# Kernel optimization log

Measured on AMD Instinct MI355X. Metric: run time of the kernel, lower is better.

The kernel has to match this reference:

```python
import jax, jax.numpy as jnp
import numpy as np
from jax import lax

DN = ('NCH', 'OIH', 'NCH')

def _conv(x, w, b, pad):
    # x: [B, C, L]; replication (edge) pad then VALID conv, per nn.ReplicationPad1d + Conv1d
    if pad != (0, 0):
        x = jnp.pad(x, ((0, 0), (0, 0), pad), mode='edge')
    y = lax.conv_general_dilated(x, w, (1,), 'VALID', dimension_numbers=DN)
    return y + b[None, :, None]

def setup_inputs() -> dict:
    key = jax.random.key(0)
    ks = jax.random.split(key, 11)
    B, L, C, H = 32, 512, 300, 512
    s = 1.0 / np.sqrt(C)
    inp = {
        'x': jax.random.normal(ks[0], (B, L, C), jnp.float32),
        'w1': jax.random.normal(ks[1], (C, C, 1), jnp.float32) * s,
        'b1': jax.random.normal(ks[2], (C,), jnp.float32) * s,
        'w2': jax.random.normal(ks[3], (C, C, 2), jnp.float32) * s,
        'b2': jax.random.normal(ks[4], (C,), jnp.float32) * s,
        'w3': jax.random.normal(ks[5], (C, C, 3), jnp.float32) * s,
        'b3': jax.random.normal(ks[6], (C,), jnp.float32) * s,
        'w7': jax.random.normal(ks[7], (C, C, 7), jnp.float32) * s,
        'b7': jax.random.normal(ks[8], (C,), jnp.float32) * s,
        'slp_w': jax.random.normal(ks[9], (H, 5 * C), jnp.float32) * (1.0 / np.sqrt(5 * C)),
        'slp_b': jax.random.normal(ks[10], (H,), jnp.float32) * (1.0 / np.sqrt(5 * C)),
    }
    return inp

def reference(x, w1, b1, w2, b2, w3, b3, w7, b7, slp_w, slp_b):
    xc = jnp.transpose(x, (0, 2, 1))  # [B, C, L]
    x1 = jnp.tanh(_conv(xc, w1, b1, (0, 0)))
    x2 = jnp.tanh(_conv(xc, w2, b2, (0, 1)))
    x3 = jnp.tanh(_conv(xc, w3, b3, (1, 1)))
    x5 = x3  # faithful to the original bug: x5 = self.conv3(x)
    x7 = jnp.tanh(_conv(xc, w7, b7, (3, 3)))
    # concat channels -> [B, L, 1500], then linear + tanh -> [B, L, 512]
    h = jnp.concatenate([x1, x2, x3, x5, x7], axis=1)  # [B, 5C, L]
    h = jnp.transpose(h, (0, 2, 1))  # [B, L, 5C]
    out = jnp.tanh(jnp.einsum('blc,hc->blh', h, slp_w) + slp_b)
    return out
```

## Files before the change

kernel.cpp:

```cpp
#include <hip/hip_runtime.h>
#include <hip/hip_bf16.h>

typedef __attribute__((ext_vector_type(8))) short short8;
typedef __attribute__((ext_vector_type(16))) float floatx16;

#define Bn 32
#define Ln 512
#define Cn 300
#define Hn 512
#define Nn (Bn*Ln)
#define XBP 518
#define XBC 320
#define HK 1216
#define LDSTC 72

#define XROWS 134
#define XSZ (XROWS*LDSTC)
#define HSROWS 128
#define HSSZ (HSROWS*LDSTC)

#define XB_ELEMS (Bn*XBP*XBC)
#define WB_ELEMS 1597440
#define WC_ELEMS (Hn*HK)
#define XB_OFF 0
#define WB_OFF (XB_OFF + XB_ELEMS)
#define WC_OFF (WB_OFF + WB_ELEMS)
#define HB_OFF (WC_OFF + WC_ELEMS)

__device__ __forceinline__ float fast_tanh(float x) {
    float ax = __builtin_fabsf(x);
    float t  = __expf(-2.f * ax);
    float r  = __builtin_fmaf(-2.f * t, __frcp_rn(1.f + t), 1.f);
    return __builtin_copysignf(r, x);
}

__device__ __forceinline__ short f2bf(float v) {
    __hip_bfloat16 h = __float2bfloat16(v);
    return *reinterpret_cast<short*>(&h);
}

__global__ void prep_all(const float* __restrict__ x,
                         const float* __restrict__ w1, const float* __restrict__ w2,
                         const float* __restrict__ w3, const float* __restrict__ w7,
                         const float* __restrict__ slp_w,
                         __hip_bfloat16* __restrict__ wsb) {
    int g = blockIdx.x * 256 + threadIdx.x;
    int idx = g * 8;
    short8 o;
    if (idx < XB_ELEMS) {
        int c8 = idx % XBC;
        int t  = idx / XBC;
        int p = t % XBP;
        int b = t / XBP;
        int l = p - 3;
        l = l < 0 ? 0 : (l > Ln - 1 ? Ln - 1 : l);
        const float* row = x + (b * Ln + l) * Cn;
        if (c8 + 8 <= Cn) {
            float4 a = *(const float4*)(row + c8);
            float4 bq = *(const float4*)(row + c8 + 4);
            o[0] = f2bf(a.x); o[1] = f2bf(a.y); o[2] = f2bf(a.z); o[3] = f2bf(a.w);
            o[4] = f2bf(bq.x); o[5] = f2bf(bq.y); o[6] = f2bf(bq.z); o[7] = f2bf(bq.w);
        } else {
#pragma unroll
            for (int e = 0; e < 8; ++e) {
                int c = c8 + e;
                o[e] = f2bf(c < Cn ? row[c] : 0.f);
            }
        }
        *(short8*)&wsb[idx] = o;
    } else if (idx < WB_OFF + WB_ELEMS) {
        int r = idx - WB_OFF, taps; const float* w;
        if (r < 122880)       { taps = 1; w = w1; }
        else if (r < 368640)  { taps = 2; w = w2; r -= 122880; }
        else if (r < 737280)  { taps = 3; w = w3; r -= 368640; }
        else                  { taps = 7; w = w7; r -= 737280; }
        int lane = (r >> 3) & 63;
        int f    = (r >> 9) & 15;
        int rt   = r >> 13;
        int t    = rt % taps;
        int mc   = rt / taps;
        int ch   = mc % 5;
        int mt   = mc / 5;
        int ks = f >> 2, mq = f & 3;
        int m = mt * 128 + mq * 32 + (lane & 31);
        int cb = ch * 64 + ks * 16 + (lane >> 5) * 8;
#pragma unroll
        for (int e = 0; e < 8; ++e) {
            int c = cb + e;
            o[e] = f2bf((m < Cn && c < Cn) ? w[(m * Cn + c) * taps + t] : 0.f);
        }
        *(short8*)&wsb[idx] = o;
    } else if (idx < WC_OFF + WC_ELEMS) {
        int r = idx - WC_OFF;
        int lane = (r >> 3) & 63;
        int f    = (r >> 9) & 15;
        int mc   = r >> 13;
        int ch   = mc % 19;
        int mt4  = mc / 19;
        int ks = f >> 2, mq = f & 3;
        int h = mt4 * 128 + mq * 32 + (lane & 31);
        int kb = ch * 64 + ks * 16 + (lane >> 5) * 8;
        const float* row = slp_w + h * 1500;
#pragma unroll
        for (int e = 0; e < 8; ++e) {
            int k = kb + e;
            float v;
            if (k < 600)       v = row[k];
            else if (k < 900)  v = row[k] + row[k + 300];
            else if (k < 1200) v = row[k + 300];
            else               v = 0.f;
            o[e] = f2bf(v);
        }
        *(short8*)&wsb[idx] = o;
    }
}

#define MFMA __builtin_amdgcn_mfma_f32_32x32x16_bf16

template<int TAPS, int LEAD>
__device__ __forceinline__ void conv_body(
        const short* __restrict__ xbs, const short* __restrict__ wsp,
        const float* __restrict__ bias, int cid, int mt, int nt,
        __hip_bfloat16* __restrict__ hbuf, short* xs) {
    const int tid  = threadIdx.x;
    const int lane = tid & 63;
    const int wave = tid >> 6;
    const int wn = wave & 1, wm = wave >> 1;
    const int lr = lane & 31;
    const int lk = (lane >> 5) << 3;
    const int TRIG = (TAPS >= 3) ? TAPS - 2 : 0;

    floatx16 acc[2][2];
#pragma unroll
    for (int i = 0; i < 2; i++)
#pragma unroll
        for (int j = 0; j < 2; j++)
#pragma unroll
            for (int r = 0; r < 16; r++) acc[i][j][r] = 0.f;

    short8 bA[8], bB[8], st[5];

#pragma unroll
    for (int i = 0; i < 5; ++i) {
        int j = tid + 256 * i;
        if (i < 4 || j < 1072)
            st[i] = *(const short8*)&xbs[(j >> 3) * XBC + ((j & 7) << 3)];
    }
#pragma unroll
    for (int ks = 0; ks < 4; ++ks)
#pragma unroll
        for (int mf = 0; mf < 2; ++mf)
            bA[ks * 2 + mf] = *(const short8*)&wsp[(ks * 4 + wm * 2 + mf) * 512 + lane * 8];
#pragma unroll
    for (int i = 0; i < 5; ++i) {
        int j = tid + 256 * i;
        if (i < 4 || j < 1072)
            *(short8*)&xs[(j >> 3) * LDSTC + ((j & 7) << 3)] = st[i];
    }
    __syncthreads();

    for (int c5 = 0; c5 < 5; ++c5) {
        const short* cur = xs + (c5 & 1) * XSZ;
        short* nxt = xs + ((c5 + 1) & 1) * XSZ;
        const int c0n = (c5 + 1) * 64;
#pragma unroll
        for (int t = 0; t < TAPS; ++t) {
            if (!(c5 == 4 && t == TAPS - 1)) {
                const short* wtn = (t + 1 < TAPS) ? wsp + (c5 * TAPS + t + 1) * 8192
                                                  : wsp + ((c5 + 1) * TAPS) * 8192;
#pragma unroll
                for (int ks = 0; ks < 4; ++ks)
#pragma unroll
                    for (int mf = 0; mf < 2; ++mf)
                        bB[ks * 2 + mf] = *(const short8*)&wtn[(ks * 4 + wm * 2 + mf) * 512 + lane * 8];
            }
            if (t == TRIG && c5 < 4) {
#pragma unroll
                for (int i = 0; i < 5; ++i) {
                    int j = tid + 256 * i;
                    if (i < 4 || j < 1072)
                        st[i] = *(const short8*)&xbs[(j >> 3) * XBC + c0n + ((j & 7) << 3)];
                }
            }
            const int sh = t - LEAD + 3;
            const int ar = (wn * 64 + lr + sh) * LDSTC + lk;
#pragma unroll
            for (int ks = 0; ks < 4; ++ks) {
                short8 a0 = *(const short8*)&cur[ar + ks * 16];
                short8 a1 = *(const short8*)&cur[ar + 32 * LDSTC + ks * 16];
                acc[0][0] = MFMA(a0, bA[ks * 2 + 0], acc[0][0], 0, 0, 0);
                acc[0][1] = MFMA(a0, bA[ks * 2 + 1], acc[0][1], 0, 0, 0);
                acc[1][0] = MFMA(a1, bA[ks * 2 + 0], acc[1][0], 0, 0, 0);
                acc[1][1] = MFMA(a1, bA[ks * 2 + 1], acc[1][1], 0, 0, 0);
            }
            if (!(c5 == 4 && t == TAPS - 1)) {
#pragma unroll
                for (int f = 0; f < 8; ++f) bA[f] = bB[f];
            }
        }
        if (c5 < 4) {
#pragma unroll
            for (int i = 0; i < 5; ++i) {
                int j = tid + 256 * i;
                if (i < 4 || j < 1072)
                    *(short8*)&nxt[(j >> 3) * LDSTC + ((j & 7) << 3)] = st[i];
            }
        }
        __syncthreads();
    }

#pragma unroll
    for (int mi = 0; mi < 2; ++mi) {
        int mloc = mt * 128 + wm * 64 + mi * 32 + lr;
        int col = cid * Cn + mloc;
        if (mloc < Cn) {
            float bv = bias[mloc];
#pragma unroll
            for (int ni = 0; ni < 2; ++ni) {
                floatx16 v = acc[ni][mi];
#pragma unroll
                for (int reg = 0; reg < 16; ++reg) {
                    int nl = wn * 64 + ni * 32 + (reg & 3) + ((reg >> 2) << 3) + ((lane >> 5) << 2);
                    int n = nt * 128 + nl;
                    hbuf[n * HK + col] = __float2bfloat16(fast_tanh(v[reg] + bv));
                }
            }
        } else if (cid == 3 && col < HK) {
            __hip_bfloat16 z = __float2bfloat16(0.f);
#pragma unroll
            for (int ni = 0; ni < 2; ++ni)
#pragma unroll
                for (int reg = 0; reg < 16; ++reg) {
                    int nl = wn * 64 + ni * 32 + (reg & 3) + ((reg >> 2) << 3) + ((lane >> 5) << 2);
                    int n = nt * 128 + nl;
                    hbuf[n * HK + col] = z;
                }
        }
    }
}

__global__ __launch_bounds__(256, 3) void conv_kernel(
        const __hip_bfloat16* __restrict__ xbg, const __hip_bfloat16* __restrict__ Wbg,
        const float* __restrict__ bias1, const float* __restrict__ bias2,
        const float* __restrict__ bias3, const float* __restrict__ bias7,
        __hip_bfloat16* __restrict__ hbuf) {
    __shared__ __align__(16) short xs[2 * XSZ];

    const int nt = blockIdx.x;
    const int y  = blockIdx.y;
    const int mt = (y >= 3) ? y - 3 : y;

    const int b  = nt >> 2;
    const int l0 = (nt & 3) << 7;
    const short* xbs = (const short*)xbg + (b * XBP + l0) * XBC;
    const short* wb  = (const short*)Wbg;

    if (y < 3) {
        conv_body<7, 3>(xbs, wb + 737280 + mt * 7 * 40960, bias7, 3, mt, nt, hbuf, xs);
        conv_body<1, 0>(xbs, wb +          mt * 1 * 40960, bias1, 0, mt, nt, hbuf, xs);
    } else {
        conv_body<3, 1>(xbs, wb + 368640 + mt * 3 * 40960, bias3, 2, mt, nt, hbuf, xs);
        conv_body<2, 0>(xbs, wb + 122880 + mt * 2 * 40960, bias2, 1, mt, nt, hbuf, xs);
    }
}

__global__ __launch_bounds__(256, 2) void linear_kernel(
        const __hip_bfloat16* __restrict__ hbufg, const __hip_bfloat16* __restrict__ Wcg,
        const float* __restrict__ slp_b, float* __restrict__ out) {
    __shared__ __align__(16) short hs[2 * HSSZ];

    const int tid  = threadIdx.x;
    const int lane = tid & 63;
    const int wave = tid >> 6;
    const int wn = wave & 1, wm = wave >> 1;
    const int lr = lane & 31;
    const int lk = (lane >> 5) << 3;

    const int nt  = blockIdx.x;
    const int mt4 = blockIdx.y;

    const short* hbp = (const short*)hbufg + nt * 128 * HK;
    const short* wcp = (const short*)Wcg + mt4 * 155648;

    floatx16 acc[2][2];
#pragma unroll
    for (int i = 0; i < 2; i++)
#pragma unroll
        for (int j = 0; j < 2; j++)
#pragma unroll
            for (int r = 0; r < 16; r++) acc[i][j][r] = 0.f;

    short8 bA[8], bB[8], st[4];

#pragma unroll
    for (int i = 0; i < 4; ++i) {
        int j = tid + 256 * i;
        st[i] = *(const short8*)&hbp[(j >> 3) * HK + ((j & 7) << 3)];
    }
#pragma unroll
    for (int ks = 0; ks < 4; ++ks)
#pragma unroll
        for (int mf = 0; mf < 2; ++mf)
            bA[ks * 2 + mf] = *(const short8*)&wcp[(ks * 4 + wm * 2 + mf) * 512 + lane * 8];
#pragma unroll
    for (int i = 0; i < 4; ++i) {
        int j = tid + 256 * i;
        *(short8*)&hs[(j >> 3) * LDSTC + ((j & 7) << 3)] = st[i];
    }
    __syncthreads();

    for (int ch = 0; ch < 19; ++ch) {
        const short* cur = hs + (ch & 1) * HSSZ;
        short* nxt = hs + ((ch + 1) & 1) * HSSZ;
        if (ch < 18) {
            const short* wtn = wcp + (ch + 1) * 8192;
#pragma unroll
            for (int ks = 0; ks < 4; ++ks)
#pragma unroll
                for (int mf = 0; mf < 2; ++mf)
                    bB[ks * 2 + mf] = *(const short8*)&wtn[(ks * 4 + wm * 2 + mf) * 512 + lane * 8];
            const int c0n = (ch + 1) * 64;
#pragma unroll
            for (int i = 0; i < 4; ++i) {
                int j = tid + 256 * i;
                st[i] = *(const short8*)&hbp[(j >> 3) * HK + c0n + ((j & 7) << 3)];
            }
        }
        const int ar = (wn * 64 + lr) * LDSTC + lk;
#pragma unroll
        for (int ks = 0; ks < 4; ++ks) {
            short8 a0 = *(const short8*)&cur[ar + ks * 16];
            short8 a1 = *(const short8*)&cur[ar + 32 * LDSTC + ks * 16];
            acc[0][0] = MFMA(a0, bA[ks * 2 + 0], acc[0][0], 0, 0, 0);
            acc[0][1] = MFMA(a0, bA[ks * 2 + 1], acc[0][1], 0, 0, 0);
            acc[1][0] = MFMA(a1, bA[ks * 2 + 0], acc[1][0], 0, 0, 0);
            acc[1][1] = MFMA(a1, bA[ks * 2 + 1], acc[1][1], 0, 0, 0);
        }
        if (ch < 18) {
#pragma unroll
            for (int f = 0; f < 8; ++f) bA[f] = bB[f];
#pragma unroll
            for (int i = 0; i < 4; ++i) {
                int j = tid + 256 * i;
                *(short8*)&nxt[(j >> 3) * LDSTC + ((j & 7) << 3)] = st[i];
            }
        }
        __syncthreads();
    }

#pragma unroll
    for (int mi = 0; mi < 2; ++mi) {
        int h = mt4 * 128 + wm * 64 + mi * 32 + lr;
        float bv = slp_b[h];
#pragma unroll
        for (int ni = 0; ni < 2; ++ni) {
            floatx16 v = acc[ni][mi];
#pragma unroll
            for (int reg = 0; reg < 16; ++reg) {
                int nl = wn * 64 + ni * 32 + (reg & 3) + ((reg >> 2) << 3) + ((lane >> 5) << 2);
                int n = nt * 128 + nl;
                out[n * Hn + h] = fast_tanh(v[reg] + bv);
            }
        }
    }
}


extern "C" void kernel_launch(void* const* d_in, const int* in_sizes, int n_in,
                              void* d_out, int out_size, void* d_ws, size_t ws_size,
                              hipStream_t stream) {
    const float* x     = (const float*)d_in[0];
    const float* w1    = (const float*)d_in[1];
    const float* b1    = (const float*)d_in[2];
    const float* w2    = (const float*)d_in[3];
    const float* b2    = (const float*)d_in[4];
    const float* w3    = (const float*)d_in[5];
    const float* b3    = (const float*)d_in[6];
    const float* w7    = (const float*)d_in[7];
    const float* b7    = (const float*)d_in[8];
    const float* slp_w = (const float*)d_in[9];
    const float* slp_b = (const float*)d_in[10];

    __hip_bfloat16* wsb = (__hip_bfloat16*)d_ws;

    const int prep_groups = (XB_ELEMS + WB_ELEMS + WC_ELEMS) / 8;
    prep_all<<<(prep_groups + 255) / 256, 256, 0, stream>>>(x, w1, w2, w3, w7, slp_w, wsb);

    conv_kernel<<<dim3(128, 6), 256, 0, stream>>>(wsb + XB_OFF, wsb + WB_OFF,
                                                  b1, b2, b3, b7, wsb + HB_OFF);
    linear_kernel<<<dim3(128, 4), 256, 0, stream>>>(wsb + HB_OFF, wsb + WC_OFF,
                                                    slp_b, (float*)d_out);
}
```

Before: 216.4 us.

## Use wide 256-channel conv tiles and split conv work per conv type across blocks

Adds a wide conv body in which each block computes 256 output channels (two M tiles, one per wave row) for one conv type. Each conv type then gets its own grid row, and the remaining channel tile runs through the original narrow body. The input tile staged in shared memory is reused across more output channels, so fewer blocks reload the same x tile. The cost is more accumulator registers, which forces launch bounds down from 3 to 2 blocks per SM, and the load across the 8 grid rows becomes uneven (7-tap versus 1-tap).

```diff
diff --git a/kernel.cpp b/kernel.cpp
--- a/kernel.cpp
+++ b/kernel.cpp
@@ -239,7 +239,110 @@
     }
 }
 
-__global__ __launch_bounds__(256, 3) void conv_kernel(
+template<int TAPS, int LEAD>
+__device__ __forceinline__ void conv_body_wide(
+        const short* __restrict__ xbs, const short* __restrict__ wsp,
+        const float* __restrict__ bias, int cid, int nt,
+        __hip_bfloat16* __restrict__ hbuf, short* xs) {
+    const int tid  = threadIdx.x;
+    const int lane = tid & 63;
+    const int wave = tid >> 6;
+    const int wn = wave & 1, wm = wave >> 1;
+    const int lr = lane & 31;
+    const int lk = (lane >> 5) << 3;
+    const int TRIG = (TAPS >= 3) ? TAPS - 2 : 0;
+    const short* wsw = wsp + wm * TAPS * 40960;
+
+    floatx16 acc[2][4];
+#pragma unroll
+    for (int i = 0; i < 2; i++)
+#pragma unroll
+        for (int j = 0; j < 4; j++)
+#pragma unroll
+            for (int r = 0; r < 16; r++) acc[i][j][r] = 0.f;
+
+    short8 bA[16], st[5];
+
+#pragma unroll
+    for (int i = 0; i < 5; ++i) {
+        int j = tid + 256 * i;
+        if (i < 4 || j < 1072)
+            st[i] = *(const short8*)&xbs[(j >> 3) * XBC + ((j & 7) << 3)];
+    }
+#pragma unroll
+    for (int f = 0; f < 16; ++f)
+        bA[f] = *(const short8*)&wsw[f * 512 + lane * 8];
+#pragma unroll
+    for (int i = 0; i < 5; ++i) {
+        int j = tid + 256 * i;
+        if (i < 4 || j < 1072)
+            *(short8*)&xs[(j >> 3) * LDSTC + ((j & 7) << 3)] = st[i];
+    }
+    __syncthreads();
+
+    for (int c5 = 0; c5 < 5; ++c5) {
+        const short* cur = xs + (c5 & 1) * XSZ;
+        short* nxt = xs + ((c5 + 1) & 1) * XSZ;
+        const int c0n = (c5 + 1) * 64;
+#pragma unroll
+        for (int t = 0; t < TAPS; ++t) {
+            if (!(c5 == 0 && t == 0)) {
+                const short* wt = wsw + (c5 * TAPS + t) * 8192;
+#pragma unroll
+                for (int f = 0; f < 16; ++f)
+                    bA[f] = *(const short8*)&wt[f * 512 + lane * 8];
+            }
+            if (t == TRIG && c5 < 4) {
+#pragma unroll
+                for (int i = 0; i < 5; ++i) {
+                    int j = tid + 256 * i;
+                    if (i < 4 || j < 1072)
+                        st[i] = *(const short8*)&xbs[(j >> 3) * XBC + c0n + ((j & 7) << 3)];
+                }
+            }
+            const int sh = t - LEAD + 3;
+            const int ar = (wn * 64 + lr + sh) * LDSTC + lk;
+#pragma unroll
+            for (int ks = 0; ks < 4; ++ks) {
+                short8 a0 = *(const short8*)&cur[ar + ks * 16];
+                short8 a1 = *(const short8*)&cur[ar + 32 * LDSTC + ks * 16];
+#pragma unroll
+                for (int mq = 0; mq < 4; ++mq) {
+                    acc[0][mq] = MFMA(a0, bA[ks * 4 + mq], acc[0][mq], 0, 0, 0);
+                    acc[1][mq] = MFMA(a1, bA[ks * 4 + mq], acc[1][mq], 0, 0, 0);
+                }
+            }
+        }
+        if (c5 < 4) {
+#pragma unroll
+            for (int i = 0; i < 5; ++i) {
+                int j = tid + 256 * i;
+                if (i < 4 || j < 1072)
+                    *(short8*)&nxt[(j >> 3) * LDSTC + ((j & 7) << 3)] = st[i];
+            }
+        }
+        __syncthreads();
+    }
+
+#pragma unroll
+    for (int mq = 0; mq < 4; ++mq) {
+        int mloc = wm * 128 + mq * 32 + lr;
+        float bv = bias[mloc];
+        int col = cid * Cn + mloc;
+#pragma unroll
+        for (int ni = 0; ni < 2; ++ni) {
+            floatx16 v = acc[ni][mq];
+#pragma unroll
+            for (int reg = 0; reg < 16; ++reg) {
+                int nl = wn * 64 + ni * 32 + (reg & 3) + ((reg >> 2) << 3) + ((lane >> 5) << 2);
+                int n = nt * 128 + nl;
+                hbuf[n * HK + col] = __float2bfloat16(fast_tanh(v[reg] + bv));
+            }
+        }
+    }
+}
+
+__global__ __launch_bounds__(256, 2) void conv_kernel(
         const __hip_bfloat16* __restrict__ xbg, const __hip_bfloat16* __restrict__ Wbg,
         const float* __restrict__ bias1, const float* __restrict__ bias2,
         const float* __restrict__ bias3, const float* __restrict__ bias7,
@@ -248,20 +351,20 @@
 
     const int nt = blockIdx.x;
     const int y  = blockIdx.y;
-    const int mt = (y >= 3) ? y - 3 : y;
 
     const int b  = nt >> 2;
     const int l0 = (nt & 3) << 7;
     const short* xbs = (const short*)xbg + (b * XBP + l0) * XBC;
     const short* wb  = (const short*)Wbg;
 
-    if (y < 3) {
-        conv_body<7, 3>(xbs, wb + 737280 + mt * 7 * 40960, bias7, 3, mt, nt, hbuf, xs);
-        conv_body<1, 0>(xbs, wb +          mt * 1 * 40960, bias1, 0, mt, nt, hbuf, xs);
-    } else {
-        conv_body<3, 1>(xbs, wb + 368640 + mt * 3 * 40960, bias3, 2, mt, nt, hbuf, xs);
-        conv_body<2, 0>(xbs, wb + 122880 + mt * 2 * 40960, bias2, 1, mt, nt, hbuf, xs);
-    }
+    if (y == 0)      conv_body_wide<7, 3>(xbs, wb + 737280, bias7, 3, nt, hbuf, xs);
+    else if (y == 1) conv_body_wide<3, 1>(xbs, wb + 368640, bias3, 2, nt, hbuf, xs);
+    else if (y == 2) conv_body_wide<2, 0>(xbs, wb + 122880, bias2, 1, nt, hbuf, xs);
+    else if (y == 3) conv_body_wide<1, 0>(xbs, wb +      0, bias1, 0, nt, hbuf, xs);
+    else if (y == 4) conv_body<7, 3>(xbs, wb + 737280 + 2 * 7 * 40960, bias7, 3, 2, nt, hbuf, xs);
+    else if (y == 5) conv_body<3, 1>(xbs, wb + 368640 + 2 * 3 * 40960, bias3, 2, 2, nt, hbuf, xs);
+    else if (y == 6) conv_body<2, 0>(xbs, wb + 122880 + 2 * 2 * 40960, bias2, 1, 2, nt, hbuf, xs);
+    else             conv_body<1, 0>(xbs, wb +      0 + 2 * 1 * 40960, bias1, 0, 2, nt, hbuf, xs);
 }
 
 __global__ __launch_bounds__(256, 2) void linear_kernel(
@@ -386,7 +489,7 @@
     const int prep_groups = (XB_ELEMS + WB_ELEMS + WC_ELEMS) / 8;
     prep_all<<<(prep_groups + 255) / 256, 256, 0, stream>>>(x, w1, w2, w3, w7, slp_w, wsb);
 
-    conv_kernel<<<dim3(128, 6), 256, 0, stream>>>(wsb + XB_OFF, wsb + WB_OFF,
+    conv_kernel<<<dim3(128, 8), 256, 0, stream>>>(wsb + XB_OFF, wsb + WB_OFF,
                                                   b1, b2, b3, b7, wsb + HB_OFF);
     linear_kernel<<<dim3(128, 4), 256, 0, stream>>>(wsb + HB_OFF, wsb + WC_OFF,
                                                     slp_b, (float*)d_out);
```

After: 218.2 us. Within noise of the previous version (+0.8%).
